# Kernel tuning notes

Hardware: AMD Instinct MI355X
Metric: run time of the kernel (lower is better)

The kernel has to match this reference:

```python
import jax, jax.numpy as jnp
import numpy as np

NH, NKV, HD = 8, 1, 256
EPS = 1e-6
SCALE = 1.0 / np.sqrt(HD)


def _rmsnorm(x, w, eps=EPS):
    # Gemma-style: normalize in fp32, scale by raw weight
    xf = x.astype(jnp.float32)
    rms = jax.lax.rsqrt(jnp.mean(xf * xf, axis=-1, keepdims=True) + eps)
    return (xf * rms).astype(x.dtype) * w


def _apply_rope(q, cos, sin):
    # q: (B, H, T, D); cos/sin: (T, D/2)
    half = q.shape[-1] // 2
    q1, q2 = q[..., :half], q[..., half:]
    c = cos[None, None, :, :]
    s = sin[None, None, :, :]
    return jnp.concatenate([q1 * c - q2 * s, q2 * c + q1 * s], axis=-1)


def setup_inputs() -> dict:
    key = jax.random.key(0)
    ks = jax.random.split(key, 8)
    B, T, H = 2, 2048, 1536
    MAXPOS, HALF = 4096, HD // 2
    x = jax.random.normal(ks[0], (B, T, H), dtype=jnp.float32)
    positions = jnp.arange(T, dtype=jnp.int64) if jax.config.jax_enable_x64 else jnp.arange(T, dtype=jnp.int32)
    # real RoPE tables
    inv_freq = 1.0 / (10000.0 ** (np.arange(0, HALF, dtype=np.float32) / HALF))
    ang = np.arange(MAXPOS, dtype=np.float32)[:, None] * inv_freq[None, :]
    cos = jnp.asarray(np.cos(ang))
    sin = jnp.asarray(np.sin(ang))
    # additive causal mask: 0 on/below diag, -1e9 above
    causal_mask = jnp.where(jnp.tril(jnp.ones((T, T), dtype=bool)), 0.0, -1e9).astype(jnp.float32)
    sc = 0.02
    Wq = jax.random.normal(ks[1], (H, NH * HD), dtype=jnp.float32) * sc
    Wk = jax.random.normal(ks[2], (H, NKV * HD), dtype=jnp.float32) * sc
    Wv = jax.random.normal(ks[3], (H, NKV * HD), dtype=jnp.float32) * sc
    Wo = jax.random.normal(ks[4], (NH * HD, H), dtype=jnp.float32) * sc
    q_norm_w = jnp.ones((HD,), dtype=jnp.float32)
    k_norm_w = jnp.ones((HD,), dtype=jnp.float32)
    return {"x": x, "positions": positions, "cos": cos, "sin": sin,
            "causal_mask": causal_mask, "Wq": Wq, "Wk": Wk, "Wv": Wv,
            "Wo": Wo, "q_norm_w": q_norm_w, "k_norm_w": k_norm_w}


def reference(x, positions, cos, sin, causal_mask, Wq, Wk, Wv, Wo, q_norm_w, k_norm_w):
    B, T, _ = x.shape
    q = (x @ Wq).reshape(B, T, NH, HD)
    k = (x @ Wk).reshape(B, T, NKV, HD)
    v = (x @ Wv).reshape(B, T, NKV, HD)
    q = _rmsnorm(q, q_norm_w)
    k = _rmsnorm(k, k_norm_w)
    q = q.transpose(0, 2, 1, 3)  # (B, NH, T, HD)
    k = k.transpose(0, 2, 1, 3)  # (B, NKV, T, HD)
    v = v.transpose(0, 2, 1, 3)
    cos_pos = cos[positions]
    sin_pos = sin[positions]
    q = _apply_rope(q, cos_pos, sin_pos)
    k = _apply_rope(k, cos_pos, sin_pos)
    if NH != NKV:
        n_rep = NH // NKV
        k = jnp.repeat(k, n_rep, axis=1)
        v = jnp.repeat(v, n_rep, axis=1)
    attn = jnp.einsum('bhqd,bhkd->bhqk', q, k) * SCALE
    attn = attn + causal_mask[None, None]
    attn = jax.nn.softmax(attn, axis=-1)
    out = jnp.einsum('bhqk,bhkd->bhqd', attn, v)
    out = out.transpose(0, 2, 1, 3).reshape(B, T, NH * HD)
    return out @ Wo
```

## Files before the change

kernel.cpp:

```cpp
#include <hip/hip_runtime.h>
#include <hip/hip_bf16.h>

typedef __bf16 bf16x8 __attribute__((ext_vector_type(8)));
typedef float  f32x4  __attribute__((ext_vector_type(4)));

__device__ __forceinline__ f32x4 mfma16(bf16x8 a, bf16x8 b, f32x4 c) {
    return __builtin_amdgcn_mfma_f32_16x16x32_bf16(a, b, c, 0, 0, 0);
}

__device__ __forceinline__ void gload_lds16(const void* g, void* l) {
    __builtin_amdgcn_global_load_lds(
        (const __attribute__((address_space(1))) void*)g,
        (__attribute__((address_space(3))) void*)l, 16, 0, 0);
}

__device__ __forceinline__ float bf2f(unsigned short u) {
    unsigned int x = (unsigned int)u << 16;
    return __builtin_bit_cast(float, x);
}
__device__ __forceinline__ unsigned short f2bf(float f) {
    return __builtin_bit_cast(unsigned short, __float2bfloat16(f));
}

#define B_   2
#define T_   2048
#define H_   1536
#define NH_  8
#define HD_  256
#define ND_  2048
#define NQKV 2560

__global__ __launch_bounds__(256) void cvt_f32_bf16(
        const float* __restrict__ src, __hip_bfloat16* __restrict__ dst, int n8) {
    int i = blockIdx.x * 256 + threadIdx.x;
    if (i >= n8) return;
    const float4* s4 = reinterpret_cast<const float4*>(src) + (size_t)i * 2;
    float4 a = s4[0], b = s4[1];
    short4 o0, o1;
    o0.x = (short)f2bf(a.x); o0.y = (short)f2bf(a.y);
    o0.z = (short)f2bf(a.z); o0.w = (short)f2bf(a.w);
    o1.x = (short)f2bf(b.x); o1.y = (short)f2bf(b.y);
    o1.z = (short)f2bf(b.z); o1.w = (short)f2bf(b.w);
    short4* d4 = reinterpret_cast<short4*>(dst) + (size_t)i * 2;
    d4[0] = o0; d4[1] = o1;
}

__global__ __launch_bounds__(256) void transpose_qkv_f32_bf16(
        const float* __restrict__ Wq, const float* __restrict__ Wk,
        const float* __restrict__ Wv, __hip_bfloat16* __restrict__ dst) {
    __shared__ float tile[32][33];
    const int bx = blockIdx.x;
    const float* src;
    int C, c0, orow0;
    if (bx < 64)      { src = Wq; C = ND_; c0 = bx * 32;        orow0 = c0; }
    else if (bx < 72) { src = Wk; C = HD_; c0 = (bx - 64) * 32; orow0 = ND_ + c0; }
    else              { src = Wv; C = HD_; c0 = (bx - 72) * 32; orow0 = ND_ + HD_ + c0; }
    const int r0 = blockIdx.y * 32;
    int tx = threadIdx.x & 31, ty = threadIdx.x >> 5;
#pragma unroll
    for (int i = 0; i < 32; i += 8)
        tile[ty + i][tx] = src[(size_t)(r0 + ty + i) * C + c0 + tx];
    __syncthreads();
#pragma unroll
    for (int i = 0; i < 32; i += 8)
        dst[(size_t)(orow0 + ty + i) * H_ + r0 + tx] =
            __float2bfloat16(tile[tx][ty + i]);
}

__global__ __launch_bounds__(256) void transpose_f32_bf16(
        const float* __restrict__ src, __hip_bfloat16* __restrict__ dst,
        int R, int C) {
    __shared__ float tile[32][33];
    int c0 = blockIdx.x * 32, r0 = blockIdx.y * 32;
    int tx = threadIdx.x & 31, ty = threadIdx.x >> 5;
#pragma unroll
    for (int i = 0; i < 32; i += 8)
        tile[ty + i][tx] = src[(size_t)(r0 + ty + i) * C + c0 + tx];
    __syncthreads();
#pragma unroll
    for (int i = 0; i < 32; i += 8)
        dst[(size_t)(c0 + ty + i) * R + r0 + tx] = __float2bfloat16(tile[tx][ty + i]);
}

__global__ __launch_bounds__(256) void transpose_bf16_s(
        const __hip_bfloat16* __restrict__ src, __hip_bfloat16* __restrict__ dst,
        int R, int C, int ss) {
    __shared__ __hip_bfloat16 tile[32][33];
    int c0 = blockIdx.x * 32, r0 = blockIdx.y * 32;
    int tx = threadIdx.x & 31, ty = threadIdx.x >> 5;
#pragma unroll
    for (int i = 0; i < 32; i += 8)
        tile[ty + i][tx] = src[(size_t)(r0 + ty + i) * ss + c0 + tx];
    __syncthreads();
#pragma unroll
    for (int i = 0; i < 32; i += 8)
        dst[(size_t)(c0 + ty + i) * R + r0 + tx] = tile[tx][ty + i];
}

template <bool F32OUT>
__global__ __launch_bounds__(256) void gemm_bt(
        const __hip_bfloat16* __restrict__ A, const __hip_bfloat16* __restrict__ Bt,
        void* __restrict__ Cp, int M, int N, int K) {
    __shared__ char smem[32768];
    const int tid  = threadIdx.x;
    const int lane = tid & 63;
    const int w    = tid >> 6;
    const int wm   = w >> 1, wn = w & 1;

    const int gx  = gridDim.x;
    const int nwg = gx * gridDim.y;
    int lin = blockIdx.x + gx * blockIdx.y;
    int swz = (lin & 7) * (nwg >> 3) + (lin >> 3);
    const int m0 = (swz / gx) * 128, n0 = (swz % gx) * 128;

    f32x4 acc[4][4] = {};

    auto STAGE = [&](int bsel, int k0) {
        char* As = smem + bsel * 16384;
        char* Bs = As + 8192;
#pragma unroll
        for (int it = 0; it < 2; ++it) {
            int o   = it * 4096 + tid * 16;
            int row = o >> 6;
            int cb  = (o & 63) ^ (((o >> 7) & 3) << 4);
            gload_lds16(A  + (size_t)(m0 + row) * K + k0 + (cb >> 1),
                        As + it * 4096 + w * 1024);
            gload_lds16(Bt + (size_t)(n0 + row) * K + k0 + (cb >> 1),
                        Bs + it * 4096 + w * 1024);
        }
    };

    const int nk = K >> 5;
    STAGE(0, 0);
    for (int ik = 0; ik < nk; ++ik) {
        if (ik + 1 < nk) {
            STAGE((ik + 1) & 1, (ik + 1) << 5);
            asm volatile("s_waitcnt vmcnt(4)" ::: "memory");
        } else {
            asm volatile("s_waitcnt vmcnt(0)" ::: "memory");
        }
        __builtin_amdgcn_s_barrier();
        __builtin_amdgcn_sched_barrier(0);

        const char* As = smem + (ik & 1) * 16384;
        const char* Bs = As + 8192;

        bf16x8 af[4], bfr[4];
#pragma unroll
        for (int i = 0; i < 4; ++i) {
            int ar = wm * 64 + i * 16 + (lane & 15);
            int q  = ar * 64 + ((lane >> 4) << 4);
            af[i]  = *(const bf16x8*)(As + (q ^ (((q >> 7) & 3) << 4)));
            int br = wn * 64 + i * 16 + (lane & 15);
            int p  = br * 64 + ((lane >> 4) << 4);
            bfr[i] = *(const bf16x8*)(Bs + (p ^ (((p >> 7) & 3) << 4)));
        }
#pragma unroll
        for (int i = 0; i < 4; ++i)
#pragma unroll
            for (int j = 0; j < 4; ++j)
                acc[i][j] = mfma16(af[i], bfr[j], acc[i][j]);

        if (ik + 1 < nk) __builtin_amdgcn_s_barrier();
    }

#pragma unroll
    for (int i = 0; i < 4; ++i) {
        int rbase = m0 + wm * 64 + i * 16 + ((lane >> 4) << 2);
#pragma unroll
        for (int j = 0; j < 4; ++j) {
            int col = n0 + wn * 64 + j * 16 + (lane & 15);
#pragma unroll
            for (int r = 0; r < 4; ++r) {
                if (F32OUT)
                    ((float*)Cp)[(size_t)(rbase + r) * N + col] = acc[i][j][r];
                else
                    ((__hip_bfloat16*)Cp)[(size_t)(rbase + r) * N + col] =
                        __float2bfloat16(acc[i][j][r]);
            }
        }
    }
}

__global__ __launch_bounds__(256) void norm_rope(
        const __hip_bfloat16* __restrict__ QKV,
        const float* __restrict__ cosT, const float* __restrict__ sinT,
        const int* __restrict__ positions,
        const float* __restrict__ qw, const float* __restrict__ kw,
        __hip_bfloat16* __restrict__ Qn, __hip_bfloat16* __restrict__ Kn) {
    int gw   = blockIdx.x * 4 + (threadIdx.x >> 6);
    int lane = threadIdx.x & 63;
    int bt   = gw / 9;
    int r    = gw - bt * 9;
    int b    = bt >> 11, t = bt & 2047;

    const __hip_bfloat16* src = QKV + (size_t)bt * NQKV + (r < 8 ? r * HD_ : ND_);
    const float* w;
    __hip_bfloat16* dst;
    float sc;
    if (r < 8) {
        w   = qw;
        dst = Qn + (((size_t)(b * NH_ + r) * T_) + t) * HD_;
        sc  = 0.0901684400555590f;
    } else {
        w   = kw;
        dst = Kn + (size_t)bt * HD_;
        sc  = 1.0f;
    }

    short4 raw = *reinterpret_cast<const short4*>(src + lane * 4);
    float v[4];
    v[0] = bf2f((unsigned short)raw.x); v[1] = bf2f((unsigned short)raw.y);
    v[2] = bf2f((unsigned short)raw.z); v[3] = bf2f((unsigned short)raw.w);

    float ss = v[0]*v[0] + v[1]*v[1] + v[2]*v[2] + v[3]*v[3];
#pragma unroll
    for (int d = 1; d < 64; d <<= 1) ss += __shfl_xor(ss, d);
    float rms = rsqrtf(ss * (1.0f / HD_) + 1e-6f);

    int pos = positions[t];
    float4 c4 = *reinterpret_cast<const float4*>(cosT + (size_t)pos * 128 + (lane & 31) * 4);
    float4 s4 = *reinterpret_cast<const float4*>(sinT + (size_t)pos * 128 + (lane & 31) * 4);
    float cv[4] = { c4.x, c4.y, c4.z, c4.w };
    float sv[4] = { s4.x, s4.y, s4.z, s4.w };

    float4 w4 = *reinterpret_cast<const float4*>(w + lane * 4);
    float wv[4] = { w4.x, w4.y, w4.z, w4.w };

    float nf[4], out[4];
#pragma unroll
    for (int j = 0; j < 4; ++j) nf[j] = v[j] * rms * wv[j];
#pragma unroll
    for (int j = 0; j < 4; ++j) {
        float pf = __shfl_xor(nf[j], 32);
        out[j] = (lane < 32) ? (nf[j] * cv[j] - pf * sv[j])
                             : (nf[j] * cv[j] + pf * sv[j]);
    }
    short4 o4;
    o4.x = (short)f2bf(out[0] * sc); o4.y = (short)f2bf(out[1] * sc);
    o4.z = (short)f2bf(out[2] * sc); o4.w = (short)f2bf(out[3] * sc);
    *reinterpret_cast<short4*>(dst + lane * 4) = o4;
}

#define NPAIR 40
__global__ __launch_bounds__(512) void flash_attn_split(
        const __hip_bfloat16* __restrict__ Qn, const __hip_bfloat16* __restrict__ Kn,
        const __hip_bfloat16* __restrict__ Vt,
        __hip_bfloat16* __restrict__ Opart, float* __restrict__ ml) {
    __shared__ char smem[2 * 16384 + 2 * 16384 + 8 * 1536];
    char* Ps = smem + 65536;

    const int tid = threadIdx.x, lane = tid & 63, wid = tid >> 6;
    const int p = blockIdx.x, bh = blockIdx.y;
    const int b = bh >> 3;

    int qt, c;
    if (p < 4)       { qt = p;                   c = 0; }
    else if (p < 12) { qt = 4 + ((p - 4) >> 1);  c = (p - 4) & 1; }
    else if (p < 24) { qt = 8 + (p - 12) / 3;    c = (p - 12) % 3; }
    else             { qt = 12 + ((p - 24) >> 2); c = (p - 24) & 3; }

    const int kv0 = c * 512;
    const int kv1 = min(kv0 + 512, (qt + 1) * 128);
    const int q0  = qt * 128 + wid * 16;
    const int nst = (kv1 - kv0) >> 5;

    const __hip_bfloat16* Qbase = Qn + ((size_t)bh * T_ + q0) * HD_;
    const __hip_bfloat16* Kb    = Kn + (size_t)b * T_ * HD_;
    const __hip_bfloat16* Vb    = Vt + (size_t)b * HD_ * T_;

    bf16x8 qf[8];
#pragma unroll
    for (int ks = 0; ks < 8; ++ks)
        qf[ks] = *(const bf16x8*)(Qbase + (size_t)(lane & 15) * HD_ + ks * 32 +
                                  ((lane >> 4) << 3));

    bf16x8 onesf;
    {
        __bf16 one = (__bf16)1.0f, zro = (__bf16)0.0f;
        __bf16 val = ((lane & 15) == 0) ? one : zro;
#pragma unroll
        for (int i = 0; i < 8; ++i) onesf[i] = val;
    }

    f32x4 acc[16] = {};
    f32x4 accl = {};

    auto STAGE = [&](int bsel, int kbb) {
        char* Kd = smem + bsel * 16384;
        char* Vd = smem + 32768 + bsel * 16384;
#pragma unroll
        for (int it = 0; it < 2; ++it) {
            int o = it * 8192 + tid * 16;
            {
                int row = o >> 9;
                int cb  = (o & 511) ^ ((row & 31) << 4);
                gload_lds16(Kb + (size_t)(kbb + row) * HD_ + (cb >> 1),
                            Kd + it * 8192 + wid * 1024);
            }
            {
                int row = o >> 6;
                int cb  = (o & 63) ^ (((o >> 7) & 3) << 4);
                gload_lds16(Vb + (size_t)row * T_ + kbb + (cb >> 1),
                            Vd + it * 8192 + wid * 1024);
            }
        }
    };

    STAGE(0, kv0);
    for (int i = 0; i < nst; ++i) {
        const int kb = kv0 + (i << 5);
        if (i + 1 < nst) {
            STAGE((i + 1) & 1, kb + 32);
            asm volatile("s_waitcnt vmcnt(4)" ::: "memory");
        } else {
            asm volatile("s_waitcnt vmcnt(0)" ::: "memory");
        }
        __builtin_amdgcn_s_barrier();
        __builtin_amdgcn_sched_barrier(0);

        const char* Ksb = smem + (i & 1) * 16384;
        const char* Vsb = smem + 32768 + (i & 1) * 16384;

        f32x4 s[2] = {};
        __builtin_amdgcn_s_setprio(1);
#pragma unroll
        for (int cf = 0; cf < 2; ++cf) {
#pragma unroll
            for (int ks = 0; ks < 8; ++ks) {
                int krow = cf * 16 + (lane & 15);
                int q    = krow * 512 + ks * 64 + ((lane >> 4) << 4);
                int sw   = q ^ (((q >> 9) & 31) << 4);
                bf16x8 kf = *(const bf16x8*)(Ksb + sw);
                s[cf] = mfma16(qf[ks], kf, s[cf]);
            }
        }
        __builtin_amdgcn_s_setprio(0);

        const bool nm = (kb + 31 > q0);
        __hip_bfloat16* pw = (__hip_bfloat16*)(Ps + wid * 1536);
#pragma unroll
        for (int r = 0; r < 4; ++r) {
            int rw = ((lane >> 4) << 2) + r;
            float s0 = s[0][r], s1 = s[1][r];
            if (nm) {
                int qrow = q0 + rw;
                if (kb + (lane & 15) > qrow)      s0 = -1e30f;
                if (kb + 16 + (lane & 15) > qrow) s1 = -1e30f;
            }
            pw[rw * 48 + (lane & 15)]      = __float2bfloat16(exp2f(s0));
            pw[rw * 48 + 16 + (lane & 15)] = __float2bfloat16(exp2f(s1));
        }

        bf16x8 pf = *(const bf16x8*)(Ps + wid * 1536 + (lane & 15) * 96 +
                                     ((lane >> 4) << 4));
        __builtin_amdgcn_s_setprio(1);
        accl = mfma16(pf, onesf, accl);
#pragma unroll
        for (int nf = 0; nf < 16; ++nf) {
            int vrow = nf * 16 + (lane & 15);
            int q    = vrow * 64 + ((lane >> 4) << 4);
            int sw   = q ^ (((q >> 7) & 3) << 4);
            bf16x8 vf = *(const bf16x8*)(Vsb + sw);
            acc[nf] = mfma16(pf, vf, acc[nf]);
        }
        __builtin_amdgcn_s_setprio(0);

        if (i + 1 < nst) __builtin_amdgcn_s_barrier();
    }

    const int slot = bh * NPAIR + p;
    __hip_bfloat16* ob = Opart + (size_t)slot * (128 * 256);
#pragma unroll
    for (int r = 0; r < 4; ++r) {
        int rw = wid * 16 + ((lane >> 4) << 2) + r;
        __hip_bfloat16* orow = ob + (size_t)rw * 256;
#pragma unroll
        for (int nf = 0; nf < 16; ++nf)
            orow[nf * 16 + (lane & 15)] = __float2bfloat16(acc[nf][r]);
        if ((lane & 15) == 0) ml[slot * 128 + rw] = accl[r];
    }
}

__global__ __launch_bounds__(256) void attn_combine(
        const __hip_bfloat16* __restrict__ Opart, const float* __restrict__ ml,
        __hip_bfloat16* __restrict__ Obuf) {
    const int bid = blockIdx.x;
    const int bh = bid >> 4, qt = bid & 15;
    const int b = bh >> 3, h = bh & 7;

    int ps, np;
    if (qt < 4)       { ps = qt;                 np = 1; }
    else if (qt < 8)  { ps = 4 + 2 * (qt - 4);   np = 2; }
    else if (qt < 12) { ps = 12 + 3 * (qt - 8);  np = 3; }
    else              { ps = 24 + 4 * (qt - 12); np = 4; }
    const int slot0 = bh * NPAIR + ps;

    const int t = threadIdx.x;
    const int row = t >> 1, half = t & 1;

    float L = 0.0f;
    for (int i = 0; i < np; ++i) L += ml[(slot0 + i) * 128 + row];
    float rL = 1.0f / L;

    __hip_bfloat16* orow = Obuf + ((size_t)(b * T_ + qt * 128 + row)) * ND_ +
                           h * HD_ + half * 128;
#pragma unroll
    for (int cc = 0; cc < 16; ++cc) {
        float a[8] = {0,0,0,0,0,0,0,0};
        for (int i = 0; i < np; ++i) {
            const __hip_bfloat16* pr = Opart + (size_t)(slot0 + i) * (128 * 256) +
                                       (size_t)row * 256 + half * 128 + cc * 8;
            short4 v0 = *reinterpret_cast<const short4*>(pr);
            short4 v1 = *reinterpret_cast<const short4*>(pr + 4);
            a[0] += bf2f((unsigned short)v0.x);
            a[1] += bf2f((unsigned short)v0.y);
            a[2] += bf2f((unsigned short)v0.z);
            a[3] += bf2f((unsigned short)v0.w);
            a[4] += bf2f((unsigned short)v1.x);
            a[5] += bf2f((unsigned short)v1.y);
            a[6] += bf2f((unsigned short)v1.z);
            a[7] += bf2f((unsigned short)v1.w);
        }
        short4 o0, o1;
        o0.x = (short)f2bf(a[0] * rL); o0.y = (short)f2bf(a[1] * rL);
        o0.z = (short)f2bf(a[2] * rL); o0.w = (short)f2bf(a[3] * rL);
        o1.x = (short)f2bf(a[4] * rL); o1.y = (short)f2bf(a[5] * rL);
        o1.z = (short)f2bf(a[6] * rL); o1.w = (short)f2bf(a[7] * rL);
        *reinterpret_cast<short4*>(orow + cc * 8)     = o0;
        *reinterpret_cast<short4*>(orow + cc * 8 + 4) = o1;
    }
}

extern "C" void kernel_launch(void* const* d_in, const int* in_sizes, int n_in,
                              void* d_out, int out_size, void* d_ws, size_t ws_size,
                              hipStream_t stream) {
    const float* x    = (const float*)d_in[0];
    const int*   pos  = (const int*)d_in[1];
    const float* cosT = (const float*)d_in[2];
    const float* sinT = (const float*)d_in[3];
    const float* Wq = (const float*)d_in[5];
    const float* Wk = (const float*)d_in[6];
    const float* Wv = (const float*)d_in[7];
    const float* Wo = (const float*)d_in[8];
    const float* qw = (const float*)d_in[9];
    const float* kw = (const float*)d_in[10];

    char* ws0 = (char*)d_ws;
    __hip_bfloat16* WqkvT  = (__hip_bfloat16*)(ws0 + 0);
    __hip_bfloat16* xb     = (__hip_bfloat16*)(ws0 + 7864320);
    __hip_bfloat16* QKVraw = (__hip_bfloat16*)(ws0 + 20447232);
    __hip_bfloat16* Opart  = (__hip_bfloat16*)(ws0 + 0);
    float*          ml     = (float*)(ws0 + 41943040);
    __hip_bfloat16* WoT    = (__hip_bfloat16*)(ws0 + 42598400);
    __hip_bfloat16* Qn     = (__hip_bfloat16*)(ws0 + 48889856);
    __hip_bfloat16* Obuf   = Qn;
    __hip_bfloat16* Kn     = (__hip_bfloat16*)(ws0 + 65667072);
    __hip_bfloat16* Vt     = (__hip_bfloat16*)(ws0 + 67764224);
    float* out = (float*)d_out;

    const int MT = B_ * T_;

    cvt_f32_bf16<<<(MT * H_ / 8 + 255) / 256, 256, 0, stream>>>(x, xb, MT * H_ / 8);

    transpose_qkv_f32_bf16<<<dim3(80, H_ / 32), 256, 0, stream>>>(
        Wq, Wk, Wv, WqkvT);
    transpose_f32_bf16<<<dim3(H_ / 32, ND_ / 32), 256, 0, stream>>>(
        Wo, WoT, ND_, H_);

    gemm_bt<false><<<dim3(NQKV / 128, MT / 128), 256, 0, stream>>>(
        xb, WqkvT, QKVraw, MT, NQKV, H_);

    norm_rope<<<(MT * 9) / 4, 256, 0, stream>>>(
        QKVraw, cosT, sinT, pos, qw, kw, Qn, Kn);

    for (int b = 0; b < B_; ++b)
        transpose_bf16_s<<<dim3(HD_ / 32, T_ / 32), 256, 0, stream>>>(
            QKVraw + (size_t)b * T_ * NQKV + ND_ + HD_,
            Vt + (size_t)b * HD_ * T_, T_, HD_, NQKV);

    flash_attn_split<<<dim3(NPAIR, B_ * NH_), 512, 0, stream>>>(
        Qn, Kn, Vt, Opart, ml);
    attn_combine<<<B_ * NH_ * 16, 256, 0, stream>>>(Opart, ml, Obuf);

    gemm_bt<true><<<dim3(H_ / 128, MT / 128), 256, 0, stream>>>(
        Obuf, WoT, out, MT, H_, ND_);
}
```

Before: 235.5 us.

## Software-pipeline attention loop: overlap next QK^T with current softmax and PV

Restructures the flash-attention KV loop into a software pipeline. The QK^T MFMAs for tile i+1 are issued before the exp/softmax and PV of tile i, so exp and LDS-store latency can overlap with matrix work. The next K/V stage load now starts after the compute of the current iteration instead of before it. This costs extra live registers for the second score tile and adds a waitcnt of zero every iteration, which may reduce the overlap of memory loads with compute.

```diff
diff --git a/kernel.cpp b/kernel.cpp
--- a/kernel.cpp
+++ b/kernel.cpp
@@ -307,23 +307,8 @@
         }
     };
 
-    STAGE(0, kv0);
-    for (int i = 0; i < nst; ++i) {
-        const int kb = kv0 + (i << 5);
-        if (i + 1 < nst) {
-            STAGE((i + 1) & 1, kb + 32);
-            asm volatile("s_waitcnt vmcnt(4)" ::: "memory");
-        } else {
-            asm volatile("s_waitcnt vmcnt(0)" ::: "memory");
-        }
-        __builtin_amdgcn_s_barrier();
-        __builtin_amdgcn_sched_barrier(0);
-
+    auto QK = [&](int i, f32x4 (&s)[2]) {
         const char* Ksb = smem + (i & 1) * 16384;
-        const char* Vsb = smem + 32768 + (i & 1) * 16384;
-
-        f32x4 s[2] = {};
-        __builtin_amdgcn_s_setprio(1);
 #pragma unroll
         for (int cf = 0; cf < 2; ++cf) {
 #pragma unroll
@@ -335,8 +320,10 @@
                 s[cf] = mfma16(qf[ks], kf, s[cf]);
             }
         }
-        __builtin_amdgcn_s_setprio(0);
-
+    };
+
+    auto SM = [&](int i, f32x4 (&s)[2]) -> bf16x8 {
+        const int kb = kv0 + (i << 5);
         const bool nm = (kb + 31 > q0);
         __hip_bfloat16* pw = (__hip_bfloat16*)(Ps + wid * 1536);
 #pragma unroll
@@ -351,10 +338,12 @@
             pw[rw * 48 + (lane & 15)]      = __float2bfloat16(exp2f(s0));
             pw[rw * 48 + 16 + (lane & 15)] = __float2bfloat16(exp2f(s1));
         }
-
-        bf16x8 pf = *(const bf16x8*)(Ps + wid * 1536 + (lane & 15) * 96 +
-                                     ((lane >> 4) << 4));
-        __builtin_amdgcn_s_setprio(1);
+        return *(const bf16x8*)(Ps + wid * 1536 + (lane & 15) * 96 +
+                                ((lane >> 4) << 4));
+    };
+
+    auto PV = [&](int i, bf16x8 pf) {
+        const char* Vsb = smem + 32768 + (i & 1) * 16384;
         accl = mfma16(pf, onesf, accl);
 #pragma unroll
         for (int nf = 0; nf < 16; ++nf) {
@@ -364,9 +353,38 @@
             bf16x8 vf = *(const bf16x8*)(Vsb + sw);
             acc[nf] = mfma16(pf, vf, acc[nf]);
         }
+    };
+
+    f32x4 sP[2] = {};
+    STAGE(0, kv0);
+    asm volatile("s_waitcnt vmcnt(0)" ::: "memory");
+    __builtin_amdgcn_s_barrier();
+    STAGE(1, kv0 + 32);
+    __builtin_amdgcn_s_setprio(1);
+    QK(0, sP);
+    __builtin_amdgcn_s_setprio(0);
+
+    for (int i = 0; i + 1 < nst; ++i) {
+        asm volatile("s_waitcnt vmcnt(0)" ::: "memory");
+        __builtin_amdgcn_s_barrier();
+        __builtin_amdgcn_sched_barrier(0);
+
+        f32x4 sN[2] = {};
+        __builtin_amdgcn_s_setprio(1);
+        QK(i + 1, sN);
+        bf16x8 pf = SM(i, sP);
+        PV(i, pf);
         __builtin_amdgcn_s_setprio(0);
 
-        if (i + 1 < nst) __builtin_amdgcn_s_barrier();
+        __builtin_amdgcn_s_barrier();
+        if (i + 2 < nst) STAGE(i & 1, kv0 + ((i + 2) << 5));
+        sP[0] = sN[0]; sP[1] = sN[1];
+    }
+    {
+        bf16x8 pf = SM(nst - 1, sP);
+        __builtin_amdgcn_s_setprio(1);
+        PV(nst - 1, pf);
+        __builtin_amdgcn_s_setprio(0);
     }
 
     const int slot = bh * NPAIR + p;
```

After: 249.5 us. +6.0%, slower.
